# Kernel optimization log

Hardware: AMD Instinct MI355X
Metric: run time of the kernel (lower is better)

Reference implementation:

```python
import jax, jax.numpy as jnp
import numpy as np

EPS = 1e-5  # config.layer_norm_epsilon

def setup_inputs() -> dict:
    key = jax.random.key(0)
    ks = jax.random.split(key, 3)
    B, S, NX, A, H, O = 16, 2048, 1024, 20, 50, 3
    x = jax.random.normal(ks[0], (B, S, NX), dtype=jnp.float32)
    ln_g = jnp.ones((A, NX), jnp.float32)
    ln_b = jnp.zeros((A, NX), jnp.float32)
    W1 = jax.random.normal(ks[1], (A, NX, H), dtype=jnp.float32) * (1.0 / np.sqrt(NX))
    b1 = jnp.zeros((A, H), jnp.float32)
    W2 = jax.random.normal(ks[2], (A, H, O), dtype=jnp.float32) * (1.0 / np.sqrt(H))
    b2 = jnp.zeros((A, O), jnp.float32)
    return {"x": x, "ln_g": ln_g, "ln_b": ln_b, "W1": W1, "b1": b1, "W2": W2, "b2": b2}

def reference(x, ln_g, ln_b, W1, b1, W2, b2):
    B, S, NX = x.shape
    A = ln_g.shape[0]
    # shared normalization (per-token mean/var), per-adapter affine folded into W1
    mu = jnp.mean(x, axis=-1, keepdims=True)
    var = jnp.mean(jnp.square(x - mu), axis=-1, keepdims=True)  # biased, like torch LN
    xn = (x - mu) * jax.lax.rsqrt(var + EPS)                    # [B,S,NX]
    W1g = ln_g[:, :, None] * W1                                 # [A,NX,H], absorbs LN gamma
    off = jnp.einsum('an,anh->ah', ln_b, W1) + b1               # [A,H],   absorbs LN beta
    h = jax.nn.relu(jnp.einsum('bsn,anh->bash', xn, W1g) + off[None, :, None, :])  # [B,A,S,H]
    o = jnp.einsum('bash,aho->baso', h, W2) + b2[None, :, None, :]                 # [B,A,S,3]
    out = o.reshape(B, A, S * o.shape[-1])                      # [B,A,S*3] (row-major == torch view)
    # squash over the adapter/capsule axis (dim=-1 of [B,S*3,A] == axis 1 here)
    sq = jnp.sum(jnp.square(out), axis=1, keepdims=True)
    scale = sq / (1.0 + sq)
    return scale * out * jax.lax.rsqrt(sq)
```

## Files before the change

kernel.cpp:

```cpp
#include <hip/hip_runtime.h>
#include <hip/hip_bf16.h>
#include <stdint.h>


typedef _Float16 h8 __attribute__((ext_vector_type(8)));
typedef float f4 __attribute__((ext_vector_type(4)));
typedef __attribute__((address_space(1))) void gvoid;
typedef __attribute__((address_space(3))) void lvoid;

__device__ __forceinline__ void cp16(const void* g, void* l) {
  __builtin_amdgcn_global_load_lds((gvoid*)g, (lvoid*)l, 16, 0, 0);
}

__global__ __launch_bounds__(256) void ln_kernel(const float* __restrict__ x,
                                                 _Float16* __restrict__ xn) {
  const int t = threadIdx.x, w = t >> 6, l = t & 63;
  const int tok = blockIdx.x * 4 + w;
  const float4* xr = (const float4*)(x + (size_t)tok * 1024);
  float4 v0 = xr[l], v1 = xr[64 + l], v2 = xr[128 + l], v3 = xr[192 + l];
  float s1 = (v0.x + v0.y + v0.z + v0.w) + (v1.x + v1.y + v1.z + v1.w) +
             (v2.x + v2.y + v2.z + v2.w) + (v3.x + v3.y + v3.z + v3.w);
  float s2 = v0.x * v0.x + v0.y * v0.y + v0.z * v0.z + v0.w * v0.w;
  s2 += v1.x * v1.x + v1.y * v1.y + v1.z * v1.z + v1.w * v1.w;
  s2 += v2.x * v2.x + v2.y * v2.y + v2.z * v2.z + v2.w * v2.w;
  s2 += v3.x * v3.x + v3.y * v3.y + v3.z * v3.z + v3.w * v3.w;
#pragma unroll
  for (int m = 32; m > 0; m >>= 1) {
    s1 += __shfl_xor(s1, m);
    s2 += __shfl_xor(s2, m);
  }
  const float mu = s1 * 0.0009765625f;
  const float var = s2 * 0.0009765625f - mu * mu;
  const float inv = rsqrtf(var + 1e-5f);
  uint2* xw = (uint2*)(xn + (size_t)tok * 1024);
  union { _Float16 h[4]; uint2 u; } q;
#define CVT_STORE(V, OFF)                                   \
  q.h[0] = (_Float16)((V.x - mu) * inv);                    \
  q.h[1] = (_Float16)((V.y - mu) * inv);                    \
  q.h[2] = (_Float16)((V.z - mu) * inv);                    \
  q.h[3] = (_Float16)((V.w - mu) * inv);                    \
  xw[(OFF) + l] = q.u;
  CVT_STORE(v0, 0)
  CVT_STORE(v1, 64)
  CVT_STORE(v2, 128)
  CVT_STORE(v3, 192)
#undef CVT_STORE
}

__global__ __launch_bounds__(256) void prep_w(const float* __restrict__ ln_g,
                                              const float* __restrict__ ln_b,
                                              const float* __restrict__ W1,
                                              _Float16* __restrict__ wB,
                                              float* __restrict__ offpart,
                                              float* __restrict__ out) {
  const int t = threadIdx.x;
  if (blockIdx.x >= 320) {
    static const int sa[7] = {2, 5, 7, 10, 12, 15, 17};
    const int idx = blockIdx.x - 320;
    const int ai = idx >> 4, bi = idx & 15;
    float4* dst = (float4*)(out + ((size_t)(bi * 20 + sa[ai])) * 6144);
    const float4 z4 = {0.f, 0.f, 0.f, 0.f};
    for (int i = t; i < 1536; i += 256) dst[i] = z4;
    return;
  }
  const int a = blockIdx.x >> 4, k0 = (blockIdx.x & 15) * 64;
  __shared__ float tw[3200];
  __shared__ float gg[64], bb[64], red[256];
  const float* src = W1 + (size_t)(a * 1024 + k0) * 50;
  for (int i = t; i < 3200; i += 256) tw[i] = src[i];
  if (t < 64) gg[t] = ln_g[a * 1024 + k0 + t];
  else if (t < 128) bb[t - 64] = ln_b[a * 1024 + k0 + (t - 64)];
  __syncthreads();
  const int h = t & 63, q = t >> 6;
  float po = 0.f;
  if (h < 50) {
#pragma unroll
    for (int half = 0; half < 2; ++half) {
      union { _Float16 hh[8]; uint4 u; } pk;
#pragma unroll
      for (int j = 0; j < 8; ++j) {
        const int k = q * 16 + half * 8 + j;
        const float wv = tw[k * 50 + h];
        pk.hh[j] = (_Float16)(gg[k] * wv);
        po += bb[k] * wv;
      }
      *(uint4*)(wB + (size_t)(a * 50 + h) * 1024 + k0 + q * 16 + half * 8) =
          pk.u;
    }
  }
  red[t] = po;
  __syncthreads();
  if (t < 50)
    offpart[(blockIdx.x & 15) * 1024 + a * 50 + t] =
        red[t] + red[64 + t] + red[128 + t] + red[192 + t];
  if (a == 0 && t < 192) {
    const uint4 z = {0, 0, 0, 0};
    *(uint4*)(wB + (size_t)(1000 + (t >> 3)) * 1024 + k0 + (t & 7) * 8) = z;
  }
}

__global__ __launch_bounds__(256, 4) void gemm_kernel(
    const _Float16* __restrict__ xn, const _Float16* __restrict__ wB,
    const float* __restrict__ offpart, const float* __restrict__ b1,
    const float* __restrict__ W2, float* __restrict__ out) {
  __shared__ __align__(16) char smem[36448];
  const int g = blockIdx.x;
  const int xcd = g & 7, i0 = g >> 3;
  const int nb = i0 & 7;
  const int mb = xcd * 32 + (i0 >> 3);
  const int t = threadIdx.x, w = t >> 6, l = t & 63;

  const int a0 = (nb * 128) / 50;
  float* w2s = (float*)(smem + 34048);
  for (int i = t; i < 600; i += 256) {
    const int j = i / 150, a = a0 + j;
    w2s[i] = (a < 20) ? W2[a * 150 + (i - j * 150)] : 0.f;
  }

  const int lr = l >> 3;
  const int ksl = (l & 7) ^ lr;
  const _Float16* gA = xn + (size_t)(mb * 128 + lr) * 1024 + ksl * 8;
  const _Float16* gB = wB + (size_t)(nb * 128 + lr) * 1024 + ksl * 8;

  const int rowA = ((w >> 1) * 64) + (l & 15);
  const int rowB = ((w & 1) * 64) + (l & 15);
  const int kq = l >> 4;
  const int xa = rowA & 7, xb = rowB & 7;
  const char* pA = smem + rowA * 128;
  const char* pB = smem + 16384 + rowB * 128;

  f4 acc[4][4];
  {
    f4 z = {0.f, 0.f, 0.f, 0.f};
#pragma unroll
    for (int mt = 0; mt < 4; ++mt)
#pragma unroll
      for (int nt = 0; nt < 4; ++nt) acc[mt][nt] = z;
  }

  for (int kt = 0; kt < 16; ++kt) {
#pragma unroll
    for (int i = 0; i < 4; ++i) {
      const int chunk = w * 4 + i;
      cp16(gA + (size_t)chunk * 8192 + kt * 64, smem + chunk * 1024);
      cp16(gB + (size_t)chunk * 8192 + kt * 64, smem + 16384 + chunk * 1024);
    }
    __syncthreads();
#pragma unroll
    for (int ks = 0; ks < 2; ++ks) {
      h8 af[4], bf[4];
      const int sl = ks * 4 + kq;
#pragma unroll
      for (int mt = 0; mt < 4; ++mt)
        af[mt] = *(const h8*)(pA + mt * 2048 + ((sl ^ xa) << 4));
#pragma unroll
      for (int nt = 0; nt < 4; ++nt)
        bf[nt] = *(const h8*)(pB + nt * 2048 + ((sl ^ xb) << 4));
#pragma unroll
      for (int mt = 0; mt < 4; ++mt)
#pragma unroll
        for (int nt = 0; nt < 4; ++nt)
          acc[mt][nt] = __builtin_amdgcn_mfma_f32_16x16x32_f16(
              af[mt], bf[nt], acc[mt][nt], 0, 0, 0);
    }
    __syncthreads();
  }

  float offt[4];
  int ncols[4];
#pragma unroll
  for (int nt = 0; nt < 4; ++nt) {
    ncols[nt] = nb * 128 + rowB + nt * 16;
    offt[nt] = (ncols[nt] < 1000) ? b1[ncols[nt]] : 0.f;
  }
#pragma unroll
  for (int c = 0; c < 16; ++c)
#pragma unroll
    for (int nt = 0; nt < 4; ++nt) offt[nt] += offpart[c * 1024 + ncols[nt]];

  const int ml = t >> 2, j = t & 3;
  const int a = a0 + j;
  const int c0 = nb * 128;
  int cs = a * 50, ce = cs + 50;
  if (cs < c0) cs = c0;
  if (ce > c0 + 128) ce = c0 + 128;
  const bool act = (a < 20) && (cs < ce);
  const int lo = cs - c0;
  const int len = act ? (ce - cs) : 0;
  const int h0 = cs - a * 50;
  const float* wrow = w2s + j * 150 + h0 * 3;

  float* hm = (float*)smem;
  const int mrl = (l >> 4) * 4;
  const int ncol = (w & 1) * 64 + (l & 15);
#pragma unroll
  for (int p = 0; p < 2; ++p) {
    if (p) __syncthreads();
    if ((w >> 1) == p) {
#pragma unroll
      for (int mt = 0; mt < 4; ++mt)
#pragma unroll
        for (int nt = 0; nt < 4; ++nt)
#pragma unroll
          for (int r = 0; r < 4; ++r)
            hm[(mrl + mt * 16 + r) * 133 + (ncol + nt * 16)] =
                fmaxf(acc[mt][nt][r] + offt[nt], 0.f);
    }
    __syncthreads();
    if (act) {
      const float* hr = hm + ml * 133 + lo;
      float o0 = 0.f, o1 = 0.f, o2 = 0.f;
      for (int i = 0; i < len; ++i) {
        const float hv = hr[i];
        o0 += hv * wrow[i * 3 + 0];
        o1 += hv * wrow[i * 3 + 1];
        o2 += hv * wrow[i * 3 + 2];
      }
      const int tok = mb * 128 + p * 64 + ml;
      const int b = tok >> 11, s = tok & 2047;
      float* op = out + ((size_t)(b * 20 + a) * 2048 + (size_t)s) * 3;
      if (len == 50) {
        op[0] = o0; op[1] = o1; op[2] = o2;
      } else {
        atomicAdd(op + 0, o0);
        atomicAdd(op + 1, o1);
        atomicAdd(op + 2, o2);
      }
    }
  }
}

__global__ __launch_bounds__(256) void squash_kernel(
    float* __restrict__ out, const float* __restrict__ b2) {
  const int idx = blockIdx.x * 256 + threadIdx.x;
  const int b = idx / 6144;
  const int rem = idx - b * 6144;
  const int oi = rem % 3;
  float v[20];
  float sq = 0.f;
#pragma unroll
  for (int a = 0; a < 20; ++a) {
    v[a] = out[((size_t)(b * 20 + a)) * 6144 + rem] + b2[a * 3 + oi];
    sq += v[a] * v[a];
  }
  const float f = sqrtf(sq) / (1.f + sq);
#pragma unroll
  for (int a = 0; a < 20; ++a)
    out[((size_t)(b * 20 + a)) * 6144 + rem] = v[a] * f;
}

extern "C" void kernel_launch(void* const* d_in, const int* in_sizes, int n_in,
                              void* d_out, int out_size, void* d_ws,
                              size_t ws_size, hipStream_t stream) {
  const float* x    = (const float*)d_in[0];
  const float* ln_g = (const float*)d_in[1];
  const float* ln_b = (const float*)d_in[2];
  const float* W1   = (const float*)d_in[3];
  const float* b1   = (const float*)d_in[4];
  const float* W2   = (const float*)d_in[5];
  const float* b2   = (const float*)d_in[6];
  float* out = (float*)d_out;

  char* ws = (char*)d_ws;
  float* offpart = (float*)ws;
  _Float16* wBw  = (_Float16*)(ws + 65536);
  _Float16* xnw  = (_Float16*)(ws + 65536 + 2097152);

  prep_w<<<432, 256, 0, stream>>>(ln_g, ln_b, W1, wBw, offpart, out);
  ln_kernel<<<8192, 256, 0, stream>>>(x, xnw);
  gemm_kernel<<<2048, 256, 0, stream>>>(xnw, wBw, offpart, b1, W2, out);
  squash_kernel<<<384, 256, 0, stream>>>(out, b2);
}
```

Baseline: 310.6 us.

## Enlarge GEMM tiles to 256x256 with double-buffered LDS and interleaved MFMA phases

The GEMM moves from 128x128 tiles with 256 threads to 256x256 tiles with 512 threads. It adds double-buffered LDS prefetch of the A and B k-slices, barrier-separated read/MFMA phases, and s_setprio hints around the MFMA bursts. This is meant to cut global reload traffic per FLOP and to hide load latency behind compute. With wider N tiles fewer adapters straddle tile boundaries, so prep_w zeroes fewer atomic-target slices. The costs are roughly 134KB of LDS per block, lower occupancy, and a grid of only 512 blocks, which may leave CUs underused.

```diff
diff --git a/kernel.cpp b/kernel.cpp
--- a/kernel.cpp
+++ b/kernel.cpp
@@ -55,7 +55,7 @@
                                               float* __restrict__ out) {
   const int t = threadIdx.x;
   if (blockIdx.x >= 320) {
-    static const int sa[7] = {2, 5, 7, 10, 12, 15, 17};
+    static const int sa[3] = {5, 10, 15};
     const int idx = blockIdx.x - 320;
     const int ai = idx >> 4, bi = idx & 15;
     float4* dst = (float4*)(out + ((size_t)(bi * 20 + sa[ai])) * 6144);
@@ -99,78 +99,165 @@
   }
 }
 
-__global__ __launch_bounds__(256, 4) void gemm_kernel(
+__global__ __launch_bounds__(512, 2) void gemm_kernel(
     const _Float16* __restrict__ xn, const _Float16* __restrict__ wB,
     const float* __restrict__ offpart, const float* __restrict__ b1,
     const float* __restrict__ W2, float* __restrict__ out) {
-  __shared__ __align__(16) char smem[36448];
+  __shared__ __align__(16) char smem[134672];
   const int g = blockIdx.x;
   const int xcd = g & 7, i0 = g >> 3;
-  const int nb = i0 & 7;
-  const int mb = xcd * 32 + (i0 >> 3);
+  const int nb = i0 & 3;
+  const int mb = xcd * 16 + (i0 >> 2);
   const int t = threadIdx.x, w = t >> 6, l = t & 63;
-
-  const int a0 = (nb * 128) / 50;
-  float* w2s = (float*)(smem + 34048);
-  for (int i = t; i < 600; i += 256) {
+  const int wr = w >> 2, wc = w & 3;
+
+  float* w2s = (float*)(smem + 131072);
+  const int a0 = (nb * 256) / 50;
+  for (int i = t; i < 900; i += 512) {
     const int j = i / 150, a = a0 + j;
     w2s[i] = (a < 20) ? W2[a * 150 + (i - j * 150)] : 0.f;
   }
 
-  const int lr = l >> 3;
-  const int ksl = (l & 7) ^ lr;
-  const _Float16* gA = xn + (size_t)(mb * 128 + lr) * 1024 + ksl * 8;
-  const _Float16* gB = wB + (size_t)(nb * 128 + lr) * 1024 + ksl * 8;
-
-  const int rowA = ((w >> 1) * 64) + (l & 15);
-  const int rowB = ((w & 1) * 64) + (l & 15);
-  const int kq = l >> 4;
-  const int xa = rowA & 7, xb = rowB & 7;
-  const char* pA = smem + rowA * 128;
-  const char* pB = smem + 16384 + rowB * 128;
-
-  f4 acc[4][4];
+  const int sr = t >> 3;
+  const int sl = (t & 7) ^ (sr & 7);
+  const _Float16* gA = xn + (size_t)(mb * 256 + sr) * 1024 + sl * 8;
+  const _Float16* gB = wB + (size_t)(nb * 256 + sr) * 1024 + sl * 8;
+  const int woff = w * 1024;
+
+  const int kq = l >> 4, xr = l & 7;
+  const char* pA0 = smem + wr * 16384 + (l & 15) * 128;
+  const char* pB0 =
+      smem + 32768 + (wc >> 1) * 16384 + ((wc & 1) * 64 + (l & 15)) * 128;
+
+  f4 acc[8][4];
   {
     f4 z = {0.f, 0.f, 0.f, 0.f};
 #pragma unroll
+    for (int mt = 0; mt < 8; ++mt)
+#pragma unroll
+      for (int nt = 0; nt < 4; ++nt) acc[mt][nt] = z;
+  }
+
+  cp16(gA, smem + woff);
+  cp16(gA + (size_t)64 * 1024, smem + 8192 + woff);
+  cp16(gA + (size_t)128 * 1024, smem + 16384 + woff);
+  cp16(gA + (size_t)192 * 1024, smem + 24576 + woff);
+  cp16(gB, smem + 32768 + woff);
+  cp16(gB + (size_t)64 * 1024, smem + 40960 + woff);
+  cp16(gB + (size_t)128 * 1024, smem + 49152 + woff);
+  cp16(gB + (size_t)192 * 1024, smem + 57344 + woff);
+  cp16(gA + 64, smem + 65536 + woff);
+  cp16(gA + (size_t)64 * 1024 + 64, smem + 65536 + 8192 + woff);
+  cp16(gA + (size_t)128 * 1024 + 64, smem + 65536 + 16384 + woff);
+  cp16(gA + (size_t)192 * 1024 + 64, smem + 65536 + 24576 + woff);
+  asm volatile("s_waitcnt vmcnt(4)" ::: "memory");
+  __builtin_amdgcn_s_barrier();
+
+#pragma unroll 2
+  for (int kt = 0; kt < 16; ++kt) {
+    const int cb = (kt & 1) << 16;
+    const int ob = cb ^ 65536;
+    h8 afA[4][2], afB[4][2], bf[4][2];
+#define RDA(mt, ks) \
+  (*(const h8*)(pA0 + cb + (mt)*2048 + ((((ks)*4 + kq) ^ xr) << 4)))
+#define RDB(nt, ks) \
+  (*(const h8*)(pB0 + cb + (nt)*2048 + ((((ks)*4 + kq) ^ xr) << 4)))
+#pragma unroll
+    for (int mt = 0; mt < 4; ++mt) {
+      afA[mt][0] = RDA(mt, 0);
+      afA[mt][1] = RDA(mt, 1);
+    }
+#pragma unroll
+    for (int nt = 0; nt < 2; ++nt) {
+      bf[nt][0] = RDB(nt, 0);
+      bf[nt][1] = RDB(nt, 1);
+    }
+    if (kt < 15) {
+      cp16(gB + (kt + 1) * 64, smem + ob + 32768 + woff);
+      cp16(gB + (size_t)64 * 1024 + (kt + 1) * 64, smem + ob + 40960 + woff);
+      cp16(gB + (size_t)128 * 1024 + (kt + 1) * 64, smem + ob + 49152 + woff);
+      cp16(gB + (size_t)192 * 1024 + (kt + 1) * 64, smem + ob + 57344 + woff);
+    }
+    __builtin_amdgcn_s_barrier();
+    asm volatile("s_waitcnt lgkmcnt(0)" ::: "memory");
+    __builtin_amdgcn_s_setprio(1);
+#pragma unroll
     for (int mt = 0; mt < 4; ++mt)
 #pragma unroll
-      for (int nt = 0; nt < 4; ++nt) acc[mt][nt] = z;
-  }
-
-  for (int kt = 0; kt < 16; ++kt) {
-#pragma unroll
-    for (int i = 0; i < 4; ++i) {
-      const int chunk = w * 4 + i;
-      cp16(gA + (size_t)chunk * 8192 + kt * 64, smem + chunk * 1024);
-      cp16(gB + (size_t)chunk * 8192 + kt * 64, smem + 16384 + chunk * 1024);
-    }
-    __syncthreads();
-#pragma unroll
-    for (int ks = 0; ks < 2; ++ks) {
-      h8 af[4], bf[4];
-      const int sl = ks * 4 + kq;
-#pragma unroll
-      for (int mt = 0; mt < 4; ++mt)
-        af[mt] = *(const h8*)(pA + mt * 2048 + ((sl ^ xa) << 4));
-#pragma unroll
-      for (int nt = 0; nt < 4; ++nt)
-        bf[nt] = *(const h8*)(pB + nt * 2048 + ((sl ^ xb) << 4));
-#pragma unroll
-      for (int mt = 0; mt < 4; ++mt)
-#pragma unroll
-        for (int nt = 0; nt < 4; ++nt)
+      for (int nt = 0; nt < 2; ++nt)
+#pragma unroll
+        for (int ks = 0; ks < 2; ++ks)
           acc[mt][nt] = __builtin_amdgcn_mfma_f32_16x16x32_f16(
-              af[mt], bf[nt], acc[mt][nt], 0, 0, 0);
-    }
-    __syncthreads();
-  }
+              afA[mt][ks], bf[nt][ks], acc[mt][nt], 0, 0, 0);
+    __builtin_amdgcn_s_setprio(0);
+    __builtin_amdgcn_s_barrier();
+#pragma unroll
+    for (int nt = 2; nt < 4; ++nt) {
+      bf[nt][0] = RDB(nt, 0);
+      bf[nt][1] = RDB(nt, 1);
+    }
+    __builtin_amdgcn_s_barrier();
+    asm volatile("s_waitcnt lgkmcnt(0)" ::: "memory");
+    __builtin_amdgcn_s_setprio(1);
+#pragma unroll
+    for (int mt = 0; mt < 4; ++mt)
+#pragma unroll
+      for (int nt = 2; nt < 4; ++nt)
+#pragma unroll
+        for (int ks = 0; ks < 2; ++ks)
+          acc[mt][nt] = __builtin_amdgcn_mfma_f32_16x16x32_f16(
+              afA[mt][ks], bf[nt][ks], acc[mt][nt], 0, 0, 0);
+    __builtin_amdgcn_s_setprio(0);
+    __builtin_amdgcn_s_barrier();
+#pragma unroll
+    for (int mt = 0; mt < 4; ++mt) {
+      afB[mt][0] = RDA(4 + mt, 0);
+      afB[mt][1] = RDA(4 + mt, 1);
+    }
+    __builtin_amdgcn_s_barrier();
+    asm volatile("s_waitcnt lgkmcnt(0)" ::: "memory");
+    __builtin_amdgcn_s_setprio(1);
+#pragma unroll
+    for (int mt = 0; mt < 4; ++mt)
+#pragma unroll
+      for (int nt = 0; nt < 2; ++nt)
+#pragma unroll
+        for (int ks = 0; ks < 2; ++ks)
+          acc[4 + mt][nt] = __builtin_amdgcn_mfma_f32_16x16x32_f16(
+              afB[mt][ks], bf[nt][ks], acc[4 + mt][nt], 0, 0, 0);
+    __builtin_amdgcn_s_setprio(0);
+    __builtin_amdgcn_s_barrier();
+    if (kt < 14) {
+      cp16(gA + (kt + 2) * 64, smem + cb + woff);
+      cp16(gA + (size_t)64 * 1024 + (kt + 2) * 64, smem + cb + 8192 + woff);
+      cp16(gA + (size_t)128 * 1024 + (kt + 2) * 64, smem + cb + 16384 + woff);
+      cp16(gA + (size_t)192 * 1024 + (kt + 2) * 64, smem + cb + 24576 + woff);
+      asm volatile("s_waitcnt vmcnt(4)" ::: "memory");
+    } else {
+      asm volatile("s_waitcnt vmcnt(0)" ::: "memory");
+    }
+    __builtin_amdgcn_s_barrier();
+    __builtin_amdgcn_s_setprio(1);
+#pragma unroll
+    for (int mt = 0; mt < 4; ++mt)
+#pragma unroll
+      for (int nt = 2; nt < 4; ++nt)
+#pragma unroll
+        for (int ks = 0; ks < 2; ++ks)
+          acc[4 + mt][nt] = __builtin_amdgcn_mfma_f32_16x16x32_f16(
+              afB[mt][ks], bf[nt][ks], acc[4 + mt][nt], 0, 0, 0);
+    __builtin_amdgcn_s_setprio(0);
+    __builtin_amdgcn_s_barrier();
+#undef RDA
+#undef RDB
+  }
+  __syncthreads();
 
   float offt[4];
   int ncols[4];
 #pragma unroll
   for (int nt = 0; nt < 4; ++nt) {
-    ncols[nt] = nb * 128 + rowB + nt * 16;
+    ncols[nt] = nb * 256 + wc * 64 + nt * 16 + (l & 15);
     offt[nt] = (ncols[nt] < 1000) ? b1[ncols[nt]] : 0.f;
   }
 #pragma unroll
@@ -178,37 +265,36 @@
 #pragma unroll
     for (int nt = 0; nt < 4; ++nt) offt[nt] += offpart[c * 1024 + ncols[nt]];
 
-  const int ml = t >> 2, j = t & 3;
+  const int ml = t >> 3, j = t & 7;
   const int a = a0 + j;
-  const int c0 = nb * 128;
+  const int c0 = nb * 256;
   int cs = a * 50, ce = cs + 50;
   if (cs < c0) cs = c0;
-  if (ce > c0 + 128) ce = c0 + 128;
-  const bool act = (a < 20) && (cs < ce);
+  if (ce > c0 + 256) ce = c0 + 256;
+  const bool act = (j < 6) && (a < 20) && (cs < ce);
   const int lo = cs - c0;
   const int len = act ? (ce - cs) : 0;
   const int h0 = cs - a * 50;
   const float* wrow = w2s + j * 150 + h0 * 3;
 
   float* hm = (float*)smem;
-  const int mrl = (l >> 4) * 4;
-  const int ncol = (w & 1) * 64 + (l & 15);
-#pragma unroll
-  for (int p = 0; p < 2; ++p) {
+#pragma unroll
+  for (int p = 0; p < 4; ++p) {
     if (p) __syncthreads();
-    if ((w >> 1) == p) {
-#pragma unroll
-      for (int mt = 0; mt < 4; ++mt)
+    if (wr == (p >> 1)) {
+      const int mtb = (p & 1) * 4;
+#pragma unroll
+      for (int q = 0; q < 4; ++q)
 #pragma unroll
         for (int nt = 0; nt < 4; ++nt)
 #pragma unroll
           for (int r = 0; r < 4; ++r)
-            hm[(mrl + mt * 16 + r) * 133 + (ncol + nt * 16)] =
-                fmaxf(acc[mt][nt][r] + offt[nt], 0.f);
+            hm[(q * 16 + kq * 4 + r) * 260 + (wc * 64 + nt * 16 + (l & 15))] =
+                fmaxf(acc[mtb + q][nt][r] + offt[nt], 0.f);
     }
     __syncthreads();
     if (act) {
-      const float* hr = hm + ml * 133 + lo;
+      const float* hr = hm + ml * 260 + lo;
       float o0 = 0.f, o1 = 0.f, o2 = 0.f;
       for (int i = 0; i < len; ++i) {
         const float hv = hr[i];
@@ -216,7 +302,7 @@
         o1 += hv * wrow[i * 3 + 1];
         o2 += hv * wrow[i * 3 + 2];
       }
-      const int tok = mb * 128 + p * 64 + ml;
+      const int tok = mb * 256 + p * 64 + ml;
       const int b = tok >> 11, s = tok & 2047;
       float* op = out + ((size_t)(b * 20 + a) * 2048 + (size_t)s) * 3;
       if (len == 50) {
@@ -266,8 +352,8 @@
   _Float16* wBw  = (_Float16*)(ws + 65536);
   _Float16* xnw  = (_Float16*)(ws + 65536 + 2097152);
 
-  prep_w<<<432, 256, 0, stream>>>(ln_g, ln_b, W1, wBw, offpart, out);
+  prep_w<<<368, 256, 0, stream>>>(ln_g, ln_b, W1, wBw, offpart, out);
   ln_kernel<<<8192, 256, 0, stream>>>(x, xnw);
-  gemm_kernel<<<2048, 256, 0, stream>>>(xnw, wBw, offpart, b1, W2, out);
+  gemm_kernel<<<512, 512, 0, stream>>>(xnw, wBw, offpart, b1, W2, out);
   squash_kernel<<<384, 256, 0, stream>>>(out, b2);
 }
```

New measurement: 307.7 us. About the same (-1.0%).
